# Kernel tuning notes

Hardware: AMD Instinct MI355X
Metric: run time of the kernel (lower is better)

## Reference

```python
import jax, jax.numpy as jnp
import numpy as np

EPS = 1e-7
PI = np.pi


def _vel_to_R(vel):
    # vel: [..., 3] -> rotation matrix [..., 3, 3] (ZY convention from spherical angles)
    rho = jnp.linalg.norm(vel, axis=-1, keepdims=True)
    theta = jnp.arctan2(vel[..., 1:2], vel[..., 0:1])
    theta = theta + (theta < 0).astype(theta.dtype) * (2.0 * PI)  # symmetric_theta=False
    phi = jnp.arccos(jnp.clip(vel[..., 2:3] / (rho + EPS), -1.0, 1.0))
    ct, st = jnp.cos(theta)[..., 0], jnp.sin(theta)[..., 0]
    cp, sp = jnp.cos(phi)[..., 0], jnp.sin(phi)[..., 0]
    z = jnp.zeros_like(ct)
    R = jnp.stack([
        jnp.stack([cp * ct, -st, sp * ct], -1),
        jnp.stack([cp * st, ct, sp * st], -1),
        jnp.stack([-sp, z, cp], -1),
    ], -2)
    return R


def _rotate(R, x):
    return jnp.einsum('...ij,...j->...i', R, x)


def setup_inputs() -> dict:
    key = jax.random.key(0)
    B, N, H, D = 128, 100, 128, 3
    in_size = 2 * D  # 6
    nef = 3 * D + D * (D - 1) // 2 + in_size  # 18 edge features
    ks = jax.random.split(key, 12)

    inputs = jax.random.normal(ks[0], (B, N, in_size), jnp.float32)

    # fully connected edges (no self loops)
    send_np, recv_np = np.nonzero(~np.eye(N, dtype=bool))
    send_edges = jnp.asarray(send_np, jnp.int32)
    recv_edges = jnp.asarray(recv_np, jnp.int32)

    def lin(k, fin, fout):
        return jax.random.normal(k, (fin, fout), jnp.float32) / np.sqrt(fin)

    return dict(
        inputs=inputs,
        W1=lin(ks[1], nef, H), b1=jnp.zeros((H,), jnp.float32),
        W2=lin(ks[2], H, H), b2=jnp.zeros((H,), jnp.float32),
        Wr=lin(ks[3], in_size, H), br=jnp.zeros((H,), jnp.float32),
        W3=lin(ks[4], H, H), b3=jnp.zeros((H,), jnp.float32),
        W4=lin(ks[5], H, H), b4=jnp.zeros((H,), jnp.float32),
        W5=lin(ks[6], H, in_size), b5=jnp.zeros((in_size,), jnp.float32),
        send_edges=send_edges, recv_edges=recv_edges,
    )


def reference(inputs, W1, b1, W2, b2, Wr, br, W3, b3, W4, b4, W5, b5,
              send_edges, recv_edges):
    D = 3
    B, N, _ = inputs.shape

    # ---- Localizer.canonicalize_inputs ----
    vel = inputs[..., D:2 * D]
    Rnode = _vel_to_R(vel)                       # [B,N,3,3]
    Rinv_node = jnp.swapaxes(Rnode, -1, -2)
    canon_vel = _rotate(Rinv_node, vel)
    rel_feat = jnp.concatenate([jnp.zeros_like(canon_vel), canon_vel], -1)  # [B,N,6]

    # ---- Localizer.create_edge_attr ----
    x_j = inputs[:, send_edges]                  # [B,E,6] senders
    x_i = inputs[:, recv_edges]                  # [B,E,6] receivers
    R = _vel_to_R(x_i[..., D:2 * D])
    R_inv = jnp.swapaxes(R, -1, -2)
    rel_pos = x_j[..., :D] - x_i[..., :D]
    rot_rel = _rotate(R_inv, rel_pos)
    send_R = _vel_to_R(x_j[..., D:2 * D])
    rot_or = R_inv @ send_R
    euler = jnp.stack([
        jnp.arctan2(rot_or[..., 1, 0], rot_or[..., 0, 0]),
        jnp.arcsin(-rot_or[..., 2, 0]),
        jnp.arctan2(rot_or[..., 2, 1], rot_or[..., 2, 2]),
    ], -1) / PI
    dist = jnp.linalg.norm(rel_pos, axis=-1, keepdims=True)
    rho_e = jnp.linalg.norm(rot_rel, axis=-1, keepdims=True)
    theta_e = jnp.arctan2(rot_rel[..., 1:2], rot_rel[..., 0:1])  # symmetric theta
    phi_e = jnp.arccos(jnp.clip(rot_rel[..., 2:3] / (rho_e + EPS), -1.0, 1.0))
    rot_vel = _rotate(R_inv, x_j[..., D:2 * D])
    edge_attr = jnp.concatenate(
        [rot_rel, euler, dist, theta_e, phi_e, rot_vel], -1)   # [B,E,12]
    edge_attr = jnp.concatenate([edge_attr, rel_feat[:, recv_edges]], -1)  # [B,E,18]

    # ---- GNN: edge MLP + scatter-mean + out MLP (dropout off in eval) ----
    h = jax.nn.silu(edge_attr @ W1 + b1) @ W2 + b2               # [B,E,H]
    agg = jnp.zeros((B, N, h.shape[-1]), h.dtype).at[:, recv_edges].add(h)
    cnt = jnp.zeros((N,), h.dtype).at[recv_edges].add(1.0)
    agg = agg / jnp.maximum(cnt, 1.0)[None, :, None]             # scatter mean
    aug = agg + rel_feat @ Wr + br
    p = jax.nn.relu(aug @ W3 + b3)
    p = jax.nn.relu(p @ W4 + b4)
    pred = p @ W5 + b5                                           # [B,N,6]

    # ---- Globalizer: rotate each 3-vector chunk back to global frame ----
    gl = jnp.concatenate(
        [_rotate(Rnode, pred[..., i:i + D]) for i in range(0, pred.shape[-1], D)], -1)
    return inputs + gl
```

## Files before the change

### kernel.cpp

```cpp
#include <hip/hip_runtime.h>
#include <math.h>

#define EPSF 1e-7f
constexpr int NN  = 100;
constexpr int DEG = 99;
constexpr int IN  = 6;
constexpr int H   = 128;
constexpr int G   = 4;
constexpr float INV_PI = 0.3183098861837907f;
constexpr float LOG2E  = 1.4426950408889634f;
constexpr float LN2    = 0.6931471805599453f;

typedef __attribute__((ext_vector_type(4))) _Float16 half4;
typedef __attribute__((ext_vector_type(8))) _Float16 half8;
typedef __attribute__((ext_vector_type(4))) float f32x4;

constexpr int XST = 144;
constexpr int SXS = 15;
constexpr int TS  = 65;
constexpr int NT  = 25;

__device__ __forceinline__ float clampf(float x, float lo, float hi) {
    return fminf(fmaxf(x, lo), hi);
}
__device__ __forceinline__ float sig2(float y) {
    return __builtin_amdgcn_rcpf(1.f + __builtin_amdgcn_exp2f(-y));
}
__device__ __forceinline__ float fast_atan2(float y, float x) {
    float ax = fabsf(x), ay = fabsf(y);
    float mx = fmaxf(ax, ay), mn = fminf(ax, ay);
    float r = mn * __builtin_amdgcn_rcpf(fmaxf(mx, 1e-35f));
    float r2 = r * r;
    float p = fmaf(r2, -0.0851330f, 0.1801410f);
    p = fmaf(r2, p, -0.3302995f);
    p = fmaf(r2, p, 0.9998660f);
    float t = r * p;
    t = (ay > ax) ? (1.5707963267948966f - t) : t;
    t = (x < 0.f) ? (3.14159265358979323f - t) : t;
    return copysignf(t, y);
}
__device__ __forceinline__ float fast_asin(float z) {
    return fast_atan2(z, sqrtf(fmaxf(0.f, (1.f - z) * (1.f + z))));
}
__device__ __forceinline__ float fast_acos(float z) {
    return fast_atan2(sqrtf(fmaxf(0.f, (1.f - z) * (1.f + z))), z);
}
__device__ __forceinline__ void vel_to_R(float vx, float vy, float vz, float* R) {
    float rho = sqrtf(vx * vx + vy * vy + vz * vz);
    float rxy = sqrtf(vx * vx + vy * vy);
    float inv = __builtin_amdgcn_rcpf(rxy);
    bool big = rxy > 1e-30f;
    float ct = big ? vx * inv : 1.f;
    float st = big ? vy * inv : 0.f;
    float cp = clampf(vz * __builtin_amdgcn_rcpf(rho + EPSF), -1.f, 1.f);
    float sp = sqrtf(fmaxf(0.f, 1.f - cp * cp));
    R[0] = cp * ct; R[1] = -st; R[2] = sp * ct;
    R[3] = cp * st; R[4] = ct;  R[5] = sp * st;
    R[6] = -sp;     R[7] = 0.f; R[8] = cp;
}

__global__ void conv_w(const float* __restrict__ W1, const float* __restrict__ W2,
                       const float* __restrict__ W3, const float* __restrict__ W4,
                       half4* __restrict__ w1f, half8* __restrict__ wmlp) {
    int t = blockIdx.x * blockDim.x + threadIdx.x;
    if (t >= 104 * 64) return;
    int L = t & 63, f = t >> 6;
    int m = L & 15, qd = L >> 4;
    if (f < 8) {
        int n = f * 16 + m;
        half4 v;
#pragma unroll
        for (int j = 0; j < 4; ++j) {
            int k = qd * 4 + j;
            v[j] = (k < 12) ? (_Float16)(W1[k * H + n] * LOG2E) : (_Float16)0.f;
        }
        w1f[f * 64 + L] = v;
    } else {
        int ff = f - 8;
        int layer = ff >> 5, rest = ff & 31;
        int kt = rest >> 3, nt = rest & 7;
        const float* W = (layer == 0) ? W2 : (layer == 1) ? W3 : W4;
        float scale = (layer == 0) ? LN2 : 1.f;
        int n = nt * 16 + m;
        half8 v;
#pragma unroll
        for (int j = 0; j < 8; ++j)
            v[j] = (_Float16)(W[(kt * 32 + qd * 8 + j) * H + n] * scale);
        wmlp[((layer * 4 + kt) * 8 + nt) * 64 + L] = v;
    }
}

__global__ __launch_bounds__(128)
void locs_fused(const float* __restrict__ in,
                const float* __restrict__ W1, const float* __restrict__ b1,
                const float* __restrict__ b2,
                const float* __restrict__ Wr, const float* __restrict__ br,
                const float* __restrict__ b3, const float* __restrict__ b4,
                const float* __restrict__ W5, const float* __restrict__ b5,
                const half4* __restrict__ w1f, const half8* __restrict__ wmlp,
                float* __restrict__ out) {
    __shared__ half4 eaA[NT * TS];
    __shared__ float sxr[NN * SXS];
    __shared__ float poolF[1056];
    __shared__ _Float16 xh[G * XST];

    float* baseF = poolF;
    float* xFp   = poolF + 512;
    float* cvF   = poolF + 1040;
    float* pbF   = poolF;
    float* predF = poolF + 384;

    const int tid = threadIdx.x;
    const int L   = tid & 63;
    const int wv  = tid >> 6;
    const int q   = L >> 4;
    const int lm  = L & 15;
    const int bn0 = blockIdx.x * G;
    const int bB  = bn0 / NN;
    const int n0  = bn0 - bB * NN;

    for (int i = tid; i < NT * TS; i += 128) eaA[i] = (half4){0, 0, 0, 0};
    if (tid < NN) {
        const float* xi = in + (bB * NN + tid) * IN;
        float R[9];
        float px = xi[0], py = xi[1], pz = xi[2];
        float vx = xi[3], vy = xi[4], vz = xi[5];
        vel_to_R(vx, vy, vz, R);
        float* dst = sxr + tid * SXS;
#pragma unroll
        for (int k = 0; k < 9; ++k) dst[k] = R[k];
        dst[9] = px; dst[10] = py; dst[11] = pz;
        dst[12] = vx; dst[13] = vy; dst[14] = vz;
    }
    __syncthreads();
    if (tid < G) {
        const float* rg = sxr + (n0 + tid) * SXS;
        float vx = rg[12], vy = rg[13], vz = rg[14];
        cvF[tid * 4 + 0] = rg[0] * vx + rg[3] * vy + rg[6] * vz;
        cvF[tid * 4 + 1] = rg[1] * vx + rg[4] * vy + rg[7] * vz;
        cvF[tid * 4 + 2] = rg[2] * vx + rg[5] * vy + rg[8] * vz;
    }
    __syncthreads();

    {
        float w15 = W1[15 * H + tid], w16 = W1[16 * H + tid], w17 = W1[17 * H + tid];
        float b1c = b1[tid];
#pragma unroll
        for (int g = 0; g < G; ++g)
            baseF[g * 128 + tid] = (b1c + cvF[g * 4 + 0] * w15
                                  + cvF[g * 4 + 1] * w16 + cvF[g * 4 + 2] * w17) * LOG2E;
    }
    half4 bfr[4];
#pragma unroll
    for (int i = 0; i < 4; ++i) bfr[i] = w1f[(wv * 4 + i) * 64 + L];

#pragma unroll
    for (int rnd = 0; rnd < 4; ++rnd) {
        int j = tid + rnd * 128;
        if (j < G * DEG) {
            int g = j / DEG;
            int e = j - g * DEG;
            int nG = n0 + g;
            int s = e < nG ? e : e + 1;
            const float* rn = sxr + nG * SXS;
            const float* rs = sxr + s * SXS;
            float Rn[9];
#pragma unroll
            for (int k = 0; k < 9; ++k) Rn[k] = rn[k];
            float rel0 = rs[9] - rn[9], rel1 = rs[10] - rn[10], rel2 = rs[11] - rn[11];
            float vjx = rs[12], vjy = rs[13], vjz = rs[14];
            float Rs0 = rs[0], Rs1 = rs[1], Rs2 = rs[2];
            float Rs3 = rs[3], Rs4 = rs[4], Rs5 = rs[5];
            float Rs6 = rs[6], Rs7 = rs[7], Rs8 = rs[8];
            float rr0 = Rn[0] * rel0 + Rn[3] * rel1 + Rn[6] * rel2;
            float rr1 = Rn[1] * rel0 + Rn[4] * rel1 + Rn[7] * rel2;
            float rr2 = Rn[2] * rel0 + Rn[5] * rel1 + Rn[8] * rel2;
            float ro00 = Rn[0] * Rs0 + Rn[3] * Rs3 + Rn[6] * Rs6;
            float ro10 = Rn[1] * Rs0 + Rn[4] * Rs3 + Rn[7] * Rs6;
            float ro20 = Rn[2] * Rs0 + Rn[5] * Rs3 + Rn[8] * Rs6;
            float ro21 = Rn[2] * Rs1 + Rn[5] * Rs4 + Rn[8] * Rs7;
            float ro22 = Rn[2] * Rs2 + Rn[5] * Rs5 + Rn[8] * Rs8;
            float dist = sqrtf(rel0 * rel0 + rel1 * rel1 + rel2 * rel2);
            half4 f0, f1, f2;
            f0[0] = (_Float16)rr0; f0[1] = (_Float16)rr1; f0[2] = (_Float16)rr2;
            f0[3] = (_Float16)(fast_atan2(ro10, ro00) * INV_PI);
            f1[0] = (_Float16)(fast_asin(clampf(-ro20, -1.f, 1.f)) * INV_PI);
            f1[1] = (_Float16)(fast_atan2(ro21, ro22) * INV_PI);
            f1[2] = (_Float16)dist;
            f1[3] = (_Float16)fast_atan2(rr1, rr0);
            f2[0] = (_Float16)fast_acos(clampf(rr2 * __builtin_amdgcn_rcpf(dist + EPSF), -1.f, 1.f));
            f2[1] = (_Float16)(Rn[0] * vjx + Rn[3] * vjy + Rn[6] * vjz);
            f2[2] = (_Float16)(Rn[1] * vjx + Rn[4] * vjy + Rn[7] * vjz);
            f2[3] = (_Float16)(Rn[2] * vjx + Rn[5] * vjy + Rn[8] * vjz);
            int t = e >> 2;
            int mrow = g * 4 + (e & 3);
            half4* dst = eaA + t * TS + mrow;
            dst[0]  = f0;
            dst[16] = f1;
            dst[32] = f2;
        }
    }
    __syncthreads();

    {
        float bs[4], part[4] = {0.f, 0.f, 0.f, 0.f};
        f32x4 c[4];
#pragma unroll
        for (int i = 0; i < 4; ++i) {
            bs[i] = baseF[q * 128 + wv * 64 + i * 16 + lm];
            c[i] = (f32x4){bs[i], bs[i], bs[i], bs[i]};
        }
#pragma unroll
        for (int t = 0; t < NT; ++t) {
            half4 a = eaA[t * TS + L];
            f32x4 d0 = __builtin_amdgcn_mfma_f32_16x16x16f16(a, bfr[0], c[0], 0, 0, 0);
            f32x4 d1 = __builtin_amdgcn_mfma_f32_16x16x16f16(a, bfr[1], c[1], 0, 0, 0);
            f32x4 d2 = __builtin_amdgcn_mfma_f32_16x16x16f16(a, bfr[2], c[2], 0, 0, 0);
            f32x4 d3 = __builtin_amdgcn_mfma_f32_16x16x16f16(a, bfr[3], c[3], 0, 0, 0);
#pragma unroll
            for (int r = 0; r < 4; ++r) {
                part[0] += d0[r] * sig2(d0[r]);
                part[1] += d1[r] * sig2(d1[r]);
                part[2] += d2[r] * sig2(d2[r]);
                part[3] += d3[r] * sig2(d3[r]);
            }
        }
#pragma unroll
        for (int i = 0; i < 4; ++i) {
            float v = part[i] - bs[i] * sig2(bs[i]);
            xFp[q * 132 + wv * 64 + i * 16 + lm] = v;
        }
    }
    __syncthreads();

#pragma unroll
    for (int layer = 0; layer < 3; ++layer) {
#pragma unroll
        for (int r = 0; r < G; ++r)
            xh[r * XST + tid] = (_Float16)xFp[r * 132 + tid];
        __syncthreads();
        int rowb = (lm & 3) * XST;
        half8 ah[4];
#pragma unroll
        for (int kt = 0; kt < 4; ++kt)
            ah[kt] = *(const half8*)&xh[rowb + kt * 32 + q * 8];
        f32x4 acc[4];
#pragma unroll
        for (int i = 0; i < 4; ++i) acc[i] = (f32x4){0.f, 0.f, 0.f, 0.f};
#pragma unroll
        for (int kt = 0; kt < 4; ++kt) {
            int base = ((layer * 4 + kt) * 8 + wv * 4) * 64 + L;
#pragma unroll
            for (int i = 0; i < 4; ++i) {
                half8 bh = wmlp[base + i * 64];
                acc[i] = __builtin_amdgcn_mfma_f32_16x16x32_f16(ah[kt], bh, acc[i], 0, 0, 0);
            }
        }
        __syncthreads();
        if (L < 16) {
#pragma unroll
            for (int i = 0; i < 4; ++i) {
                int ch = wv * 64 + i * 16 + lm;
                if (layer == 0) {
                    float b2c = b2[ch], brc = br[ch];
                    float w3c = Wr[3 * H + ch], w4c = Wr[4 * H + ch], w5c = Wr[5 * H + ch];
#pragma unroll
                    for (int r = 0; r < 4; ++r)
                        xFp[r * 132 + ch] = acc[i][r] * (1.f / 99.f) + b2c
                                          + cvF[r * 4 + 0] * w3c + cvF[r * 4 + 1] * w4c
                                          + cvF[r * 4 + 2] * w5c + brc;
                } else {
                    float bb = (layer == 1) ? b3[ch] : b4[ch];
#pragma unroll
                    for (int r = 0; r < 4; ++r)
                        xFp[r * 132 + ch] = fmaxf(0.f, acc[i][r] + bb);
                }
            }
        }
        __syncthreads();
    }

    if (tid < 96) {
        int o = tid >> 4, sl = tid & 15, kb = sl * 8;
        float w5[8];
#pragma unroll
        for (int j = 0; j < 8; ++j) w5[j] = W5[(kb + j) * IN + o];
#pragma unroll
        for (int g = 0; g < G; ++g) {
            float s = 0.f;
#pragma unroll
            for (int j = 0; j < 8; ++j) s = fmaf(xFp[g * 132 + kb + j], w5[j], s);
            pbF[g * 96 + sl * 6 + o] = s;
        }
    }
    __syncthreads();
    if (tid < 24) {
        int g = tid / 6, o = tid - g * 6;
        float s = b5[o];
#pragma unroll
        for (int sl = 0; sl < 16; ++sl) s += pbF[g * 96 + sl * 6 + o];
        predF[g * 8 + o] = s;
    }
    __syncthreads();
    if (tid < 24) {
        int g = tid / 6, o = tid - g * 6;
        int r = (o < 3) ? o : o - 3;
        int off = (o < 3) ? 0 : 3;
        const float* Rg = sxr + (n0 + g) * SXS;
        float gl = Rg[r * 3 + 0] * predF[g * 8 + off + 0]
                 + Rg[r * 3 + 1] * predF[g * 8 + off + 1]
                 + Rg[r * 3 + 2] * predF[g * 8 + off + 2];
        int bng = bn0 + g;
        out[bng * IN + o] = Rg[9 + o] + gl;
    }
}

extern "C" void kernel_launch(void* const* d_in, const int* in_sizes, int n_in,
                              void* d_out, int out_size, void* d_ws, size_t ws_size,
                              hipStream_t stream) {
    const float* in = (const float*)d_in[0];
    const float* W1 = (const float*)d_in[1];
    const float* b1 = (const float*)d_in[2];
    const float* W2 = (const float*)d_in[3];
    const float* b2 = (const float*)d_in[4];
    const float* Wr = (const float*)d_in[5];
    const float* br = (const float*)d_in[6];
    const float* W3 = (const float*)d_in[7];
    const float* b3 = (const float*)d_in[8];
    const float* W4 = (const float*)d_in[9];
    const float* b4 = (const float*)d_in[10];
    const float* W5 = (const float*)d_in[11];
    const float* b5 = (const float*)d_in[12];
    float* out = (float*)d_out;

    half4* w1f  = (half4*)d_ws;
    half8* wmlp = (half8*)((char*)d_ws + 4096);

    const int BN = in_sizes[0] / IN;
    conv_w<<<26, 256, 0, stream>>>(W1, W2, W3, W4, w1f, wmlp);
    locs_fused<<<BN / G, 128, 0, stream>>>(in, W1, b1, b2, Wr, br, b3, b4,
                                           W5, b5, w1f, wmlp, out);
}
```

Baseline: 144.6 us.

## Shrink LDS footprint and compute edge-MLP bias in registers

Shrinks the edge-feature tile stride from 65 to 50 by mapping the fourth lane quad onto a single shared zero row, instead of keeping separate zero-padded rows. The xh buffer now aliases that half-precision pool, which cuts shared memory per block. The layer-1 bias is computed directly in registers from global weights rather than staged through LDS, removing one barrier. The aim is more resident blocks per CU and fewer synchronizations, at the cost of a denser LDS access pattern that may cause bank conflicts.

```diff
diff --git a/kernel.cpp b/kernel.cpp
--- a/kernel.cpp
+++ b/kernel.cpp
@@ -17,7 +17,7 @@
 
 constexpr int XST = 144;
 constexpr int SXS = 15;
-constexpr int TS  = 65;
+constexpr int TS  = 50;
 constexpr int NT  = 25;
 
 __device__ __forceinline__ float clampf(float x, float lo, float hi) {
@@ -99,16 +99,12 @@
                 const float* __restrict__ W5, const float* __restrict__ b5,
                 const half4* __restrict__ w1f, const half8* __restrict__ wmlp,
                 float* __restrict__ out) {
-    __shared__ half4 eaA[NT * TS];
+    __shared__ _Float16 hpool[NT * TS * 4];
     __shared__ float sxr[NN * SXS];
-    __shared__ float poolF[1056];
-    __shared__ _Float16 xh[G * XST];
-
-    float* baseF = poolF;
-    float* xFp   = poolF + 512;
-    float* cvF   = poolF + 1040;
-    float* pbF   = poolF;
-    float* predF = poolF + 384;
+    __shared__ float xFp[G * 132];
+    __shared__ float cvF[16];
+    __shared__ float pbF[G * 96];
+    __shared__ float predF[G * 8];
 
     const int tid = threadIdx.x;
     const int L   = tid & 63;
@@ -119,7 +115,10 @@
     const int bB  = bn0 / NN;
     const int n0  = bn0 - bB * NN;
 
-    for (int i = tid; i < NT * TS; i += 128) eaA[i] = (half4){0, 0, 0, 0};
+    {
+        half4 z = {0, 0, 0, 0};
+        for (int i = tid; i < NT * TS; i += 128) *(half4*)&hpool[i * 4] = z;
+    }
     if (tid < NN) {
         const float* xi = in + (bB * NN + tid) * IN;
         float R[9];
@@ -139,16 +138,6 @@
         cvF[tid * 4 + 0] = rg[0] * vx + rg[3] * vy + rg[6] * vz;
         cvF[tid * 4 + 1] = rg[1] * vx + rg[4] * vy + rg[7] * vz;
         cvF[tid * 4 + 2] = rg[2] * vx + rg[5] * vy + rg[8] * vz;
-    }
-    __syncthreads();
-
-    {
-        float w15 = W1[15 * H + tid], w16 = W1[16 * H + tid], w17 = W1[17 * H + tid];
-        float b1c = b1[tid];
-#pragma unroll
-        for (int g = 0; g < G; ++g)
-            baseF[g * 128 + tid] = (b1c + cvF[g * 4 + 0] * w15
-                                  + cvF[g * 4 + 1] * w16 + cvF[g * 4 + 2] * w17) * LOG2E;
     }
     half4 bfr[4];
 #pragma unroll
@@ -194,25 +183,34 @@
             f2[3] = (_Float16)(Rn[2] * vjx + Rn[5] * vjy + Rn[8] * vjz);
             int t = e >> 2;
             int mrow = g * 4 + (e & 3);
-            half4* dst = eaA + t * TS + mrow;
-            dst[0]  = f0;
-            dst[16] = f1;
-            dst[32] = f2;
-        }
-    }
-    __syncthreads();
-
+            _Float16* dst = hpool + (t * TS + mrow) * 4;
+            *(half4*)(dst +   0)      = f0;
+            *(half4*)(dst + 16 * 4)   = f1;
+            *(half4*)(dst + 32 * 4)   = f2;
+        }
+    }
+
+    float bs[4];
     {
-        float bs[4], part[4] = {0.f, 0.f, 0.f, 0.f};
+        float cv0 = cvF[q * 4 + 0], cv1 = cvF[q * 4 + 1], cv2 = cvF[q * 4 + 2];
+#pragma unroll
+        for (int i = 0; i < 4; ++i) {
+            int ch = wv * 64 + i * 16 + lm;
+            bs[i] = (b1[ch] + cv0 * W1[15 * H + ch] + cv1 * W1[16 * H + ch]
+                   + cv2 * W1[17 * H + ch]) * LOG2E;
+        }
+    }
+    __syncthreads();
+
+    {
+        float part[4] = {0.f, 0.f, 0.f, 0.f};
         f32x4 c[4];
 #pragma unroll
-        for (int i = 0; i < 4; ++i) {
-            bs[i] = baseF[q * 128 + wv * 64 + i * 16 + lm];
-            c[i] = (f32x4){bs[i], bs[i], bs[i], bs[i]};
-        }
+        for (int i = 0; i < 4; ++i) c[i] = (f32x4){bs[i], bs[i], bs[i], bs[i]};
+        const int loff = (q < 3) ? (q * 16 + lm) : 48;
 #pragma unroll
         for (int t = 0; t < NT; ++t) {
-            half4 a = eaA[t * TS + L];
+            half4 a = *(const half4*)&hpool[(t * TS + loff) * 4];
             f32x4 d0 = __builtin_amdgcn_mfma_f32_16x16x16f16(a, bfr[0], c[0], 0, 0, 0);
             f32x4 d1 = __builtin_amdgcn_mfma_f32_16x16x16f16(a, bfr[1], c[1], 0, 0, 0);
             f32x4 d2 = __builtin_amdgcn_mfma_f32_16x16x16f16(a, bfr[2], c[2], 0, 0, 0);
@@ -226,13 +224,12 @@
             }
         }
 #pragma unroll
-        for (int i = 0; i < 4; ++i) {
-            float v = part[i] - bs[i] * sig2(bs[i]);
-            xFp[q * 132 + wv * 64 + i * 16 + lm] = v;
-        }
-    }
-    __syncthreads();
-
+        for (int i = 0; i < 4; ++i)
+            xFp[q * 132 + wv * 64 + i * 16 + lm] = part[i] - bs[i] * sig2(bs[i]);
+    }
+    __syncthreads();
+
+    _Float16* xh = hpool;
 #pragma unroll
     for (int layer = 0; layer < 3; ++layer) {
 #pragma unroll
```

Result: no change. 142.8 us (-1.2%).
